# Optimization experiments

Hardware: AMD Instinct MI355X
Metric: run time of the kernel (lower is better)

Reference implementation:

```python
import jax, jax.numpy as jnp
import numpy as np

N = 50000      # nodes
E = 400000     # edges (before self-loops)
IN = 128       # in_channels
OUT = 64       # out_channels (per-head; concat=False averages heads)
HEADS = 8      # heads of first GAT layer; second layer has 1 head
NEG_SLOPE = 0.2


def _glorot(key, shape, fan_in, fan_out):
    s = jnp.sqrt(2.0 / (fan_in + fan_out)).astype(jnp.float32)
    return jax.random.normal(key, shape, jnp.float32) * s


def setup_inputs() -> dict:
    key = jax.random.key(0)
    ks = jax.random.split(key, 10)
    x = jax.random.normal(ks[0], (N, IN), jnp.float32)
    edge_index = jax.random.randint(ks[1], (2, E), 0, N)
    # layer 1: heads=HEADS, per-head dim OUT
    W1 = _glorot(ks[2], (IN, HEADS * OUT), IN, HEADS * OUT)
    att_src1 = _glorot(ks[3], (HEADS, OUT), OUT, 1)
    att_dst1 = _glorot(ks[4], (HEADS, OUT), OUT, 1)
    b1 = jnp.zeros((OUT,), jnp.float32)
    # layer 2: heads=1
    W2 = _glorot(ks[5], (OUT, 1 * OUT), OUT, OUT)
    att_src2 = _glorot(ks[6], (1, OUT), OUT, 1)
    att_dst2 = _glorot(ks[7], (1, OUT), OUT, 1)
    b2 = jnp.zeros((OUT,), jnp.float32)
    return dict(x=x, edge_index=edge_index, W1=W1, att_src1=att_src1,
                att_dst1=att_dst1, b1=b1, W2=W2, att_src2=att_src2,
                att_dst2=att_dst2, b2=b2)


def gat_conv(x, edge_index, W, att_src, att_dst, bias, heads, ch):
    """PyG GATConv with concat=False (mean over heads), add_self_loops=True."""
    n = x.shape[0]
    loop = jnp.arange(n, dtype=edge_index.dtype)
    src = jnp.concatenate([edge_index[0], loop])  # [E+N]
    dst = jnp.concatenate([edge_index[1], loop])
    h = (x @ W).reshape(n, heads, ch)                     # [N, H, C]
    a_s = jnp.sum(h * att_src, axis=-1)                   # [N, H]
    a_d = jnp.sum(h * att_dst, axis=-1)                   # [N, H]
    e = jax.nn.leaky_relu(a_s[src] + a_d[dst], NEG_SLOPE)  # [E+N, H]
    # numerically stable segment softmax over incoming edges of each dst node
    emax = jax.lax.stop_gradient(
        jax.ops.segment_max(e, dst, num_segments=n))       # [N, H]
    ee = jnp.exp(e - emax[dst])
    denom = jax.ops.segment_sum(ee, dst, num_segments=n)  # [N, H]
    alpha = ee / denom[dst]                                # [E+N, H]
    out = jax.ops.segment_sum(alpha[:, :, None] * h[src], dst,
                              num_segments=n)              # [N, H, C]
    return out.mean(axis=1) + bias                         # [N, C]


def reference(x, edge_index, W1, att_src1, att_dst1, b1,
              W2, att_src2, att_dst2, b2):
    h = gat_conv(x, edge_index, W1, att_src1, att_dst1, b1, HEADS, OUT)
    h = jax.nn.elu(h)
    return gat_conv(h, edge_index, W2, att_src2, att_dst2, b2, 1, OUT)
```

## Files before the change

kernel.cpp:

```cpp
#include <hip/hip_runtime.h>
#include <cstdint>
#include <cstddef>

#define NEG_SLOPE 0.2f

typedef short bf16x8 __attribute__((ext_vector_type(8)));
typedef float f32x4 __attribute__((ext_vector_type(4)));
typedef float f32x2 __attribute__((ext_vector_type(2)));

__device__ __forceinline__ unsigned short f2bf(float f) {
  unsigned u = __float_as_uint(f);
  u = u + 0x7FFFu + ((u >> 16) & 1u);
  return (unsigned short)(u >> 16);
}
__device__ __forceinline__ float bf2f(unsigned short b) {
  return __uint_as_float((unsigned)b << 16);
}
__device__ __forceinline__ f32x2 unpk(unsigned xv) {
  f32x2 r;
  r.x = __uint_as_float(xv << 16);
  r.y = __uint_as_float(xv & 0xFFFF0000u);
  return r;
}
__device__ __forceinline__ float rlf(float v, int l) {
  return __uint_as_float(
      (unsigned)__builtin_amdgcn_readlane((int)__float_as_uint(v), l));
}
__device__ __forceinline__ void dma16(const unsigned short* g, unsigned short* l) {
  __builtin_amdgcn_global_load_lds(
      (const __attribute__((address_space(1))) unsigned*)g,
      (__attribute__((address_space(3))) unsigned*)l, 16, 0, 0);
}

__global__ __launch_bounds__(256) void prep_all(
    const int* __restrict__ ei, int* __restrict__ counts,
    const float* __restrict__ x, unsigned short* __restrict__ xb,
    const float* __restrict__ W1, const float* __restrict__ att_s1,
    const float* __restrict__ att_d1, unsigned short* __restrict__ AsAdT,
    unsigned short* __restrict__ WbT,
    const float* __restrict__ W2, unsigned short* __restrict__ W2t,
    const float* __restrict__ att_s2, const float* __restrict__ att_d2,
    float* __restrict__ AsAd2,
    int E, int ET, int N, int B0, int B1) {
  int b = blockIdx.x, tid = threadIdx.x;
  if (b < B0) {
    int i = b * 256 + tid;
    if (i < ET) {
      int dst = (i < E) ? ei[E + i] : (i - E);
      atomicAdd(&counts[dst], 1);
    }
    return;
  }
  b -= B0;
  if (b < B1) {
    int i = b * 256 + tid;
    if (i < N * 32) {
      float4 v = ((const float4*)x)[i];
      ushort4 o;
      o.x = f2bf(v.x); o.y = f2bf(v.y); o.z = f2bf(v.z); o.w = f2bf(v.w);
      ((ushort4*)xb)[i] = o;
    }
    return;
  }
  b -= B1;
  if (b < 8) {
    int i = b * 256 + tid;
    int o = i >> 7, k = i & 127, h = o & 7;
    const float* att = (o < 8) ? att_s1 : att_d1;
    float s = 0.f;
    for (int c = 0; c < 64; c++) s += W1[(size_t)k * 512 + h * 64 + c] * att[h * 64 + c];
    AsAdT[i] = f2bf(s);
    return;
  }
  b -= 8;
  if (b < 256) {
    int i = b * 256 + tid;
    int o = i >> 10, k = i & 1023, h = k >> 7, c = k & 127;
    WbT[i] = f2bf(W1[(size_t)c * 512 + h * 64 + o]);
    return;
  }
  b -= 256;
  if (b < 16) {
    int i = b * 256 + tid;
    if (i < 64 * 64) {
      int k = i >> 6, nn = i & 63;
      W2t[(size_t)nn * 64 + k] = f2bf(W2[i]);
    }
    return;
  }
  {
    int i = tid;
    if (i < 128) {
      int o = i >> 6, k = i & 63;
      const float* att = (o == 0) ? att_s2 : att_d2;
      float s = 0.f;
      for (int c = 0; c < 64; c++) s += W2[(size_t)k * 64 + c] * att[c];
      AsAd2[i] = s;
    }
  }
}

__global__ __launch_bounds__(1024) void scan_dots(
    const int* __restrict__ counts, int* __restrict__ offsets,
    const unsigned short* __restrict__ xb, const unsigned short* __restrict__ AsAdT,
    float* __restrict__ asd, int n) {
  if (blockIdx.x == 0) {
    __shared__ int sums[1024];
    int t = threadIdx.x;
    int chunk = (n + 1023) >> 10;
    int start = t * chunk;
    int end = min(start + chunk, n);
    int s = 0;
    for (int i = start; i < end; i++) s += counts[i];
    sums[t] = s;
    __syncthreads();
    for (int off = 1; off < 1024; off <<= 1) {
      int v = (t >= off) ? sums[t - off] : 0;
      __syncthreads();
      sums[t] += v;
      __syncthreads();
    }
    int run = sums[t] - s;
    for (int i = start; i < end; i++) { offsets[i] = run; run += counts[i]; }
    if (t == 1023) offsets[n] = sums[1023];
    return;
  }
  int tid = threadIdx.x;
  int wave = tid >> 6, lane = tid & 63;
  int q = lane >> 4, t = lane & 15;
  int row0 = (blockIdx.x - 1) * 256 + wave * 16;
  int arow = row0 + t; if (arow > n - 1) arow = n - 1;
  const bf16x8* aptr = (const bf16x8*)(xb + (size_t)arow * 128);
  const bf16x8* bptr = (const bf16x8*)(AsAdT + t * 128);
  f32x4 acc = (f32x4){0.f, 0.f, 0.f, 0.f};
  #pragma unroll
  for (int s = 0; s < 4; s++)
    acc = __builtin_amdgcn_mfma_f32_16x16x32_bf16(aptr[s * 4 + q], bptr[s * 4 + q],
                                                  acc, 0, 0, 0);
  #pragma unroll
  for (int r = 0; r < 4; r++) {
    int row = row0 + q * 4 + r;
    if (row < n) asd[row * 16 + t] = acc[r];
  }
}

__global__ __launch_bounds__(256) void fill_csr(
    const int* __restrict__ ei, const int* __restrict__ offsets,
    int* __restrict__ cursor, int* __restrict__ srcs, int E, int ET) {
  int i = blockIdx.x * 256 + threadIdx.x;
  if (i >= ET) return;
  int src, dst;
  if (i < E) { src = ei[i]; dst = ei[E + i]; } else { src = dst = i - E; }
  int pos = atomicAdd(&cursor[dst], 1);
  srcs[offsets[dst] + pos] = src;
}

__global__ __launch_bounds__(1024, 8) void agg1_gemm(
    const int* __restrict__ offsets, const int* __restrict__ srcs,
    const float* __restrict__ asd, const unsigned short* __restrict__ xb,
    const unsigned short* __restrict__ WbT, const float* __restrict__ b1,
    const float* __restrict__ AsAd2, unsigned short* __restrict__ zb,
    float* __restrict__ as2, float* __restrict__ ad2, int N) {
  __shared__ unsigned short sh[16 * 2048];
  int tid = threadIdx.x;
  int wv = tid >> 6, lane = tid & 63;
  int nb = blockIdx.x;
  {
    int node = nb * 16 + wv;
    unsigned short* stg = &sh[wv * 2048];
    f32x2 acc[8];
    #pragma unroll
    for (int h = 0; h < 8; h++) acc[h] = (f32x2){0.f, 0.f};
    float wsl = 0.f;
    int beg = offsets[node], end = offsets[node + 1];
    int jl = end - 1;
    float adv = asd[(size_t)node * 16 + 8 + (lane & 7)];
    int s0 = srcs[min(beg + (lane >> 4), jl)];
    int s1 = srcs[min(beg + 4 + (lane >> 4), jl)];
    int s2 = 0, s3 = 0;
    float asva, asvb = 0.f;
    {
      int swa = srcs[min(beg + (lane >> 3), jl)];
      asva = asd[(size_t)swa * 16 + (lane & 7)];
    }
    if (end - beg > 8) {
      s2 = srcs[min(beg + 8 + (lane >> 4), jl)];
      s3 = srcs[min(beg + 12 + (lane >> 4), jl)];
      int swb = srcs[min(beg + 8 + (lane >> 3), jl)];
      asvb = asd[(size_t)swb * 16 + (lane & 7)];
    }
    for (int cb = beg; cb < end; cb += 16) {
      int rem = end - cb;
      bool bigh = rem > 8;
      dma16(xb + (size_t)s0 * 128 + (lane & 15) * 8, stg);
      dma16(xb + (size_t)s1 * 128 + (lane & 15) * 8, stg + 512);
      if (bigh) {
        dma16(xb + (size_t)s2 * 128 + (lane & 15) * 8, stg + 1024);
        dma16(xb + (size_t)s3 * 128 + (lane & 15) * 8, stg + 1536);
      }
      float wa, wb = 0.f;
      {
        float v = asva + adv;
        v = (v > 0.f) ? v : NEG_SLOPE * v;
        wa = (cb + (lane >> 3) < end) ? __expf(v) : 0.f;
      }
      if (bigh) {
        float v = asvb + adv;
        v = (v > 0.f) ? v : NEG_SLOPE * v;
        wb = (cb + 8 + (lane >> 3) < end) ? __expf(v) : 0.f;
      }
      wsl += wa + wb;
      int cn = cb + 16;
      if (cn < end) {
        s0 = srcs[min(cn + (lane >> 4), jl)];
        s1 = srcs[min(cn + 4 + (lane >> 4), jl)];
        int swa = srcs[min(cn + (lane >> 3), jl)];
        asva = asd[(size_t)swa * 16 + (lane & 7)];
        if (end - cn > 8) {
          s2 = srcs[min(cn + 8 + (lane >> 4), jl)];
          s3 = srcs[min(cn + 12 + (lane >> 4), jl)];
          int swb = srcs[min(cn + 8 + (lane >> 3), jl)];
          asvb = asd[(size_t)swb * 16 + (lane & 7)];
        }
      }
      __builtin_amdgcn_s_waitcnt(0x0f70);
      #pragma unroll
      for (int k = 0; k < 8; k++) {
        unsigned xv = *(const unsigned*)&stg[k * 128 + 2 * lane];
        f32x2 x2 = unpk(xv);
        acc[0] += x2 * rlf(wa, k * 8 + 0);
        acc[1] += x2 * rlf(wa, k * 8 + 1);
        acc[2] += x2 * rlf(wa, k * 8 + 2);
        acc[3] += x2 * rlf(wa, k * 8 + 3);
        acc[4] += x2 * rlf(wa, k * 8 + 4);
        acc[5] += x2 * rlf(wa, k * 8 + 5);
        acc[6] += x2 * rlf(wa, k * 8 + 6);
        acc[7] += x2 * rlf(wa, k * 8 + 7);
      }
      if (bigh) {
        #pragma unroll
        for (int k = 0; k < 8; k++) {
          unsigned xv = *(const unsigned*)&stg[1024 + k * 128 + 2 * lane];
          f32x2 x2 = unpk(xv);
          acc[0] += x2 * rlf(wb, k * 8 + 0);
          acc[1] += x2 * rlf(wb, k * 8 + 1);
          acc[2] += x2 * rlf(wb, k * 8 + 2);
          acc[3] += x2 * rlf(wb, k * 8 + 3);
          acc[4] += x2 * rlf(wb, k * 8 + 4);
          acc[5] += x2 * rlf(wb, k * 8 + 5);
          acc[6] += x2 * rlf(wb, k * 8 + 6);
          acc[7] += x2 * rlf(wb, k * 8 + 7);
        }
      }
    }
    wsl += __shfl_xor(wsl, 8, 64);
    wsl += __shfl_xor(wsl, 16, 64);
    wsl += __shfl_xor(wsl, 32, 64);
    __syncthreads();
    #pragma unroll
    for (int h = 0; h < 8; h++) {
      float tot = rlf(wsl, h);
      float iv = 0.125f / tot;
      unsigned o = (unsigned)f2bf(acc[h].x * iv) | ((unsigned)f2bf(acc[h].y * iv) << 16);
      *(unsigned*)&sh[wv * 1032 + h * 128 + 2 * lane] = o;
    }
  }
  __syncthreads();
  if (wv < 4) {
    int q = lane >> 4, t = lane & 15;
    f32x4 acc4 = (f32x4){0.f, 0.f, 0.f, 0.f};
    const unsigned short* bbase = WbT + (size_t)(wv * 16 + t) * 1024;
    #pragma unroll 8
    for (int s = 0; s < 32; s++) {
      bf16x8 af = *(const bf16x8*)&sh[t * 1032 + s * 32 + q * 8];
      bf16x8 bf = *(const bf16x8*)&bbase[s * 32 + q * 8];
      acc4 = __builtin_amdgcn_mfma_f32_16x16x32_bf16(af, bf, acc4, 0, 0, 0);
    }
    int col = wv * 16 + t;
    float bias = b1[col];
    float vs = AsAd2[col], vd = AsAd2[64 + col];
    #pragma unroll
    for (int r = 0; r < 4; r++) {
      int row = q * 4 + r;
      int node = nb * 16 + row;
      float v = acc4[r] + bias;
      v = (v > 0.f) ? v : (__expf(v) - 1.f);
      zb[(size_t)node * 64 + col] = f2bf(v);
      float s = v * vs, d = v * vd;
      #pragma unroll
      for (int off = 1; off < 16; off <<= 1) {
        s += __shfl_xor(s, off, 64);
        d += __shfl_xor(d, off, 64);
      }
      if (t == 0) {
        atomicAdd(&as2[node], s);
        atomicAdd(&ad2[node], d);
      }
    }
  }
}

__global__ __launch_bounds__(1024, 8) void agg2_gemm(
    const int* __restrict__ offsets, const int* __restrict__ srcs,
    const float* __restrict__ as2, const float* __restrict__ ad2,
    const unsigned short* __restrict__ zb, const unsigned short* __restrict__ W2t,
    const float* __restrict__ b2, float* __restrict__ out, int N) {
  __shared__ unsigned short stg[16 * 1024];
  __shared__ unsigned short sh[16 * 72];
  int tid = threadIdx.x;
  int wv = tid >> 6, lane = tid & 63;
  int nb = blockIdx.x;
  {
    int node = nb * 16 + wv;
    unsigned short* st = &stg[wv * 1024];
    float adv = ad2[node];
    int beg = offsets[node], end = offsets[node + 1];
    int jl = end - 1;
    f32x2 acc = (f32x2){0.f, 0.f};
    float wsl = 0.f;
    for (int cb = beg; cb < end; cb += 16) {
      int s0 = srcs[min(cb + (lane >> 3), jl)];
      int s1 = srcs[min(cb + 8 + (lane >> 3), jl)];
      int we = srcs[min(cb + (lane & 15), jl)];
      float asv = as2[we];
      dma16(zb + (size_t)s0 * 64 + (lane & 7) * 8, st);
      dma16(zb + (size_t)s1 * 64 + (lane & 7) * 8, st + 512);
      float v = asv + adv;
      v = (v > 0.f) ? v : NEG_SLOPE * v;
      float wl = (cb + (lane & 15) < end) ? __expf(v) : 0.f;
      if (lane < 16) wsl += wl;
      __builtin_amdgcn_s_waitcnt(0x0f70);
      #pragma unroll
      for (int k = 0; k < 8; k++) {
        float w0 = rlf(wl, 2 * k);
        float w1 = rlf(wl, 2 * k + 1);
        float w = (lane >= 32) ? w1 : w0;
        unsigned zv = *(const unsigned*)&st[(2 * k + (lane >> 5)) * 64 + 2 * (lane & 31)];
        acc += unpk(zv) * w;
      }
    }
    wsl += __shfl_xor(wsl, 1, 64);
    wsl += __shfl_xor(wsl, 2, 64);
    wsl += __shfl_xor(wsl, 4, 64);
    wsl += __shfl_xor(wsl, 8, 64);
    float tot = rlf(wsl, 0);
    acc.x += __shfl_xor(acc.x, 32, 64);
    acc.y += __shfl_xor(acc.y, 32, 64);
    if (lane < 32) {
      float inv = 1.f / tot;
      unsigned o = (unsigned)f2bf(acc.x * inv) | ((unsigned)f2bf(acc.y * inv) << 16);
      *(unsigned*)&sh[wv * 72 + 2 * lane] = o;
    }
  }
  __syncthreads();
  if (wv < 4) {
    int q = lane >> 4, t = lane & 15;
    f32x4 acc4 = (f32x4){0.f, 0.f, 0.f, 0.f};
    const unsigned short* bbase = W2t + (size_t)(wv * 16 + t) * 64;
    #pragma unroll
    for (int s = 0; s < 2; s++) {
      bf16x8 af = *(const bf16x8*)&sh[t * 72 + s * 32 + q * 8];
      bf16x8 bf = *(const bf16x8*)&bbase[s * 32 + q * 8];
      acc4 = __builtin_amdgcn_mfma_f32_16x16x32_bf16(af, bf, acc4, 0, 0, 0);
    }
    int col = wv * 16 + t;
    float bias = b2[col];
    #pragma unroll
    for (int r = 0; r < 4; r++) {
      int node = nb * 16 + q * 4 + r;
      if (node < N) out[(size_t)node * 64 + col] = acc4[r] + bias;
    }
  }
}

extern "C" void kernel_launch(void* const* d_in, const int* in_sizes, int n_in,
                              void* d_out, int out_size, void* d_ws, size_t ws_size,
                              hipStream_t stream) {
  const int IN = 128;
  const int N = in_sizes[0] / IN;
  const int E = in_sizes[1] / 2;
  const int ET = E + N;

  const float* x        = (const float*)d_in[0];
  const int*   ei       = (const int*)d_in[1];
  const float* W1       = (const float*)d_in[2];
  const float* att_src1 = (const float*)d_in[3];
  const float* att_dst1 = (const float*)d_in[4];
  const float* b1       = (const float*)d_in[5];
  const float* W2       = (const float*)d_in[6];
  const float* att_src2 = (const float*)d_in[7];
  const float* att_dst2 = (const float*)d_in[8];
  const float* b2       = (const float*)d_in[9];
  float* out = (float*)d_out;

  char* base = (char*)d_ws;
  size_t off = 0;
  auto alloc = [&](size_t bytes) -> char* {
    char* p = base + off;
    off = (off + bytes + 255) & ~(size_t)255;
    return p;
  };
  unsigned short* xb    = (unsigned short*)alloc((size_t)N * 128 * 2);
  unsigned short* AsAdT = (unsigned short*)alloc((size_t)16 * 128 * 2);
  unsigned short* WbT   = (unsigned short*)alloc((size_t)64 * 1024 * 2);
  unsigned short* W2t   = (unsigned short*)alloc((size_t)64 * 64 * 2);
  unsigned short* zb    = (unsigned short*)alloc((size_t)N * 64 * 2);
  float* AsAd2 = (float*)alloc((size_t)128 * 4);
  float* asd1  = (float*)alloc((size_t)N * 16 * 4);
  int* offsets = (int*)alloc((size_t)(N + 1) * 4);
  int* srcs    = (int*)alloc((size_t)ET * 4);
  char* zero_begin = base + off;
  int* counts  = (int*)alloc((size_t)N * 4);
  int* cursor  = (int*)alloc((size_t)N * 4);
  float* a_s2  = (float*)alloc((size_t)N * 4);
  float* a_d2  = (float*)alloc((size_t)N * 4);
  char* zero_end = base + off;

  hipMemsetAsync(zero_begin, 0, (size_t)(zero_end - zero_begin), stream);

  const int TB = 256;
  auto cdiv = [](int a, int b) { return (a + b - 1) / b; };

  int B0 = cdiv(ET, TB);
  int B1 = cdiv(N * 32, TB);
  prep_all<<<B0 + B1 + 8 + 256 + 16 + 1, TB, 0, stream>>>(
      ei, counts, x, xb, W1, att_src1, att_dst1, AsAdT, WbT, W2, W2t,
      att_src2, att_dst2, AsAd2, E, ET, N, B0, B1);

  scan_dots<<<1 + cdiv(N, 256), 1024, 0, stream>>>(counts, offsets, xb, AsAdT,
                                                   asd1, N);

  fill_csr<<<cdiv(ET, TB), TB, 0, stream>>>(ei, offsets, cursor, srcs, E, ET);

  agg1_gemm<<<cdiv(N, 16), 1024, 0, stream>>>(offsets, srcs, asd1, xb, WbT, b1,
                                              AsAd2, zb, a_s2, a_d2, N);

  agg2_gemm<<<cdiv(N, 16), 1024, 0, stream>>>(offsets, srcs, a_s2, a_d2, zb,
                                              W2t, b2, out, N);
}
```

Before: 326.3 us.

## Gather neighbor rows with per-edge 4-byte LDS DMA and skip padded edges

Both aggregation kernels now gather source rows with one 4-byte global-to-LDS load per lane per edge (one full row per wave instruction, source index broadcast via readlane). Edges past the segment end are skipped instead of loaded with clamped indices. The staging buffers are zeroed once so skipped slots hold zero. The cross-iteration prefetch of srcs and attention scores is removed, so index loads are now serialized with the gathers in each chunk, and many more smaller DMA instructions are issued.

```diff
diff --git a/kernel.cpp b/kernel.cpp
--- a/kernel.cpp
+++ b/kernel.cpp
@@ -30,6 +30,11 @@
   __builtin_amdgcn_global_load_lds(
       (const __attribute__((address_space(1))) unsigned*)g,
       (__attribute__((address_space(3))) unsigned*)l, 16, 0, 0);
+}
+__device__ __forceinline__ void dma4(const unsigned short* g, unsigned short* l) {
+  __builtin_amdgcn_global_load_lds(
+      (const __attribute__((address_space(1))) unsigned*)g,
+      (__attribute__((address_space(3))) unsigned*)l, 4, 0, 0);
 }
 
 __global__ __launch_bounds__(256) void prep_all(
@@ -168,6 +173,10 @@
   {
     int node = nb * 16 + wv;
     unsigned short* stg = &sh[wv * 2048];
+    #pragma unroll
+    for (int z = 0; z < 4; z++)
+      ((f32x4*)stg)[z * 64 + lane] = (f32x4){0.f, 0.f, 0.f, 0.f};
+    __builtin_amdgcn_s_waitcnt(0xC07F);
     f32x2 acc[8];
     #pragma unroll
     for (int h = 0; h < 8; h++) acc[h] = (f32x2){0.f, 0.f};
@@ -175,28 +184,19 @@
     int beg = offsets[node], end = offsets[node + 1];
     int jl = end - 1;
     float adv = asd[(size_t)node * 16 + 8 + (lane & 7)];
-    int s0 = srcs[min(beg + (lane >> 4), jl)];
-    int s1 = srcs[min(beg + 4 + (lane >> 4), jl)];
-    int s2 = 0, s3 = 0;
-    float asva, asvb = 0.f;
-    {
-      int swa = srcs[min(beg + (lane >> 3), jl)];
-      asva = asd[(size_t)swa * 16 + (lane & 7)];
-    }
-    if (end - beg > 8) {
-      s2 = srcs[min(beg + 8 + (lane >> 4), jl)];
-      s3 = srcs[min(beg + 12 + (lane >> 4), jl)];
-      int swb = srcs[min(beg + 8 + (lane >> 3), jl)];
-      asvb = asd[(size_t)swb * 16 + (lane & 7)];
-    }
     for (int cb = beg; cb < end; cb += 16) {
-      int rem = end - cb;
-      bool bigh = rem > 8;
-      dma16(xb + (size_t)s0 * 128 + (lane & 15) * 8, stg);
-      dma16(xb + (size_t)s1 * 128 + (lane & 15) * 8, stg + 512);
-      if (bigh) {
-        dma16(xb + (size_t)s2 * 128 + (lane & 15) * 8, stg + 1024);
-        dma16(xb + (size_t)s3 * 128 + (lane & 15) * 8, stg + 1536);
+      int cnt = min(16, end - cb);
+      int sAll = srcs[min(cb + (lane & 15), jl)];
+      int swa = srcs[min(cb + (lane >> 3), jl)];
+      int swb = srcs[min(cb + 8 + (lane >> 3), jl)];
+      float asva = asd[(size_t)swa * 16 + (lane & 7)];
+      float asvb = asd[(size_t)swb * 16 + (lane & 7)];
+      #pragma unroll
+      for (int k = 0; k < 16; k++) {
+        if (k < cnt) {
+          int se = __builtin_amdgcn_readlane(sAll, k);
+          dma4(xb + (size_t)(unsigned)se * 128 + 2 * lane, stg + k * 128);
+        }
       }
       float wa, wb = 0.f;
       {
@@ -204,25 +204,12 @@
         v = (v > 0.f) ? v : NEG_SLOPE * v;
         wa = (cb + (lane >> 3) < end) ? __expf(v) : 0.f;
       }
-      if (bigh) {
+      if (cnt > 8) {
         float v = asvb + adv;
         v = (v > 0.f) ? v : NEG_SLOPE * v;
         wb = (cb + 8 + (lane >> 3) < end) ? __expf(v) : 0.f;
       }
       wsl += wa + wb;
-      int cn = cb + 16;
-      if (cn < end) {
-        s0 = srcs[min(cn + (lane >> 4), jl)];
-        s1 = srcs[min(cn + 4 + (lane >> 4), jl)];
-        int swa = srcs[min(cn + (lane >> 3), jl)];
-        asva = asd[(size_t)swa * 16 + (lane & 7)];
-        if (end - cn > 8) {
-          s2 = srcs[min(cn + 8 + (lane >> 4), jl)];
-          s3 = srcs[min(cn + 12 + (lane >> 4), jl)];
-          int swb = srcs[min(cn + 8 + (lane >> 3), jl)];
-          asvb = asd[(size_t)swb * 16 + (lane & 7)];
-        }
-      }
       __builtin_amdgcn_s_waitcnt(0x0f70);
       #pragma unroll
       for (int k = 0; k < 8; k++) {
@@ -237,7 +224,7 @@
         acc[6] += x2 * rlf(wa, k * 8 + 6);
         acc[7] += x2 * rlf(wa, k * 8 + 7);
       }
-      if (bigh) {
+      if (cnt > 8) {
         #pragma unroll
         for (int k = 0; k < 8; k++) {
           unsigned xv = *(const unsigned*)&stg[1024 + k * 128 + 2 * lane];
@@ -313,30 +300,50 @@
   {
     int node = nb * 16 + wv;
     unsigned short* st = &stg[wv * 1024];
+    #pragma unroll
+    for (int z = 0; z < 2; z++)
+      ((f32x4*)st)[z * 64 + lane] = (f32x4){0.f, 0.f, 0.f, 0.f};
+    __builtin_amdgcn_s_waitcnt(0xC07F);
     float adv = ad2[node];
     int beg = offsets[node], end = offsets[node + 1];
     int jl = end - 1;
     f32x2 acc = (f32x2){0.f, 0.f};
     float wsl = 0.f;
     for (int cb = beg; cb < end; cb += 16) {
-      int s0 = srcs[min(cb + (lane >> 3), jl)];
-      int s1 = srcs[min(cb + 8 + (lane >> 3), jl)];
-      int we = srcs[min(cb + (lane & 15), jl)];
-      float asv = as2[we];
-      dma16(zb + (size_t)s0 * 64 + (lane & 7) * 8, st);
-      dma16(zb + (size_t)s1 * 64 + (lane & 7) * 8, st + 512);
+      int cnt = min(16, end - cb);
+      int sAll = srcs[min(cb + (lane & 15), jl)];
+      float asv = as2[sAll];
+      #pragma unroll
+      for (int k = 0; k < 8; k++) {
+        if (2 * k < cnt) {
+          int sa = __builtin_amdgcn_readlane(sAll, 2 * k);
+          int sb = __builtin_amdgcn_readlane(sAll, 2 * k + 1);
+          int se = (lane >= 32) ? sb : sa;
+          dma4(zb + (size_t)(unsigned)se * 64 + 2 * (lane & 31), st + k * 128);
+        }
+      }
       float v = asv + adv;
       v = (v > 0.f) ? v : NEG_SLOPE * v;
       float wl = (cb + (lane & 15) < end) ? __expf(v) : 0.f;
       if (lane < 16) wsl += wl;
       __builtin_amdgcn_s_waitcnt(0x0f70);
       #pragma unroll
-      for (int k = 0; k < 8; k++) {
+      for (int k = 0; k < 4; k++) {
         float w0 = rlf(wl, 2 * k);
         float w1 = rlf(wl, 2 * k + 1);
         float w = (lane >= 32) ? w1 : w0;
-        unsigned zv = *(const unsigned*)&st[(2 * k + (lane >> 5)) * 64 + 2 * (lane & 31)];
+        unsigned zv = *(const unsigned*)&st[k * 128 + 2 * lane];
         acc += unpk(zv) * w;
+      }
+      if (cnt > 8) {
+        #pragma unroll
+        for (int k = 4; k < 8; k++) {
+          float w0 = rlf(wl, 2 * k);
+          float w1 = rlf(wl, 2 * k + 1);
+          float w = (lane >= 32) ? w1 : w0;
+          unsigned zv = *(const unsigned*)&st[k * 128 + 2 * lane];
+          acc += unpk(zv) * w;
+        }
       }
     }
     wsl += __shfl_xor(wsl, 1, 64);
```

Result: slower. 347.7 us (+6.6%).
